# Optimization experiments

Measured on AMD Instinct MI355X. Metric: run time of the kernel, lower is better.

The kernel has to match this reference:

```python
import jax, jax.numpy as jnp
import numpy as np

B, Himg, Wimg, DIM = 8, 128, 128, 256
HEADS = 16            # d_head = DIM // HEADS = 16 == HEADS (required by temperature broadcast)
HW = Himg * Wimg


def setup_inputs() -> dict:
    key = jax.random.key(0)
    ks = jax.random.split(key, 9)
    s = 0.02
    return {
        "x": jax.random.normal(ks[0], (B, Himg, Wimg, DIM), jnp.float32),
        "w_qkv": jax.random.normal(ks[1], (DIM, 3 * DIM), jnp.float32) * s,
        "w_dw": jax.random.normal(ks[2], (3, 3, 1, 3 * DIM), jnp.float32) * s,  # HWIO, depthwise
        "w_out": jax.random.normal(ks[3], (DIM, DIM), jnp.float32) * s,
        "temperature": jnp.ones((1, 1, HEADS), jnp.float32),
        "mean_q": jax.random.normal(ks[4], (1, 1, HW, 1), jnp.float32) * 0.05,
        "var_q": 0.5 + jax.random.uniform(ks[5], (1, 1, HW, 1), jnp.float32),
        "mean_k": jax.random.normal(ks[6], (1, 1, HW, 1), jnp.float32) * 0.05,
        "var_k": 0.5 + jax.random.uniform(ks[7], (1, 1, HW, 1), jnp.float32),
    }


def _to_heads(t, b, hw, heads):
    # (b,h,w,heads*dh) -> (b, heads, h*w, dh)
    return t.reshape(b, hw, heads, -1).transpose(0, 2, 1, 3)


def reference(x, w_qkv, w_dw, w_out, temperature, mean_q, var_q, mean_k, var_k):
    b, h, w, c = x.shape
    heads = temperature.shape[-1]
    # pointwise QKV projection (1x1 conv, no bias)
    qkv = jnp.einsum('bhwc,cd->bhwd', x, w_qkv)
    # depthwise 3x3 conv, groups = 3*dim, 'same' padding
    qkv = jax.lax.conv_general_dilated(
        qkv, w_dw, window_strides=(1, 1), padding='SAME',
        dimension_numbers=('NHWC', 'HWIO', 'NHWC'),
        feature_group_count=3 * c)
    q, k, v = jnp.split(qkv, 3, axis=-1)
    q = _to_heads(q, b, h * w, heads)  # (b, heads, hw, dh)
    k = _to_heads(k, b, h * w, heads)
    v = _to_heads(v, b, h * w, heads)
    # keras Normalization(axis=-2): per-spatial-position mean/variance
    q = (q - mean_q) * jax.lax.rsqrt(var_q)
    k = (k - mean_k) * jax.lax.rsqrt(var_k)
    # channel attention: k^T @ q over spatial axis -> (b, heads, dh, dh)
    attn = jnp.einsum('bnsi,bnsj->bnij', k, q)
    attn = attn * temperature  # broadcasts over last axis (dh == heads)
    attn = jax.nn.softmax(attn, axis=-2)
    out = jnp.einsum('bnsd,bndj->bnsj', v, attn)  # v @ attn
    # (b, heads, hw, dh) -> (b, h, w, heads*dh)
    out = out.transpose(0, 2, 1, 3).reshape(b, h, w, c)
    out = jnp.einsum('bhwc,cd->bhwd', out, w_out)
    return out
```

## Files before the change

kernel.cpp:

```cpp
#include <hip/hip_runtime.h>
#include <cstdint>
#include <cstddef>

#define NB    8
#define HWSZ  16384
#define DIM   256
#define NCH   128
#define CHSZ  (HWSZ / NCH)

typedef short bf16x8 __attribute__((ext_vector_type(8)));
typedef float f32x4 __attribute__((ext_vector_type(4)));
typedef unsigned short u16;
typedef u16 u16x8 __attribute__((ext_vector_type(8)));

__device__ __forceinline__ float bf2f(u16 u) {
    union { uint32_t i; float f; } w; w.i = ((uint32_t)u) << 16; return w.f;
}
__device__ __forceinline__ u16 f2bf(float f) {
    union { float f; uint32_t i; } w; w.f = f;
    uint32_t x = w.i;
    return (u16)((x + 0x7fffu + ((x >> 16) & 1u)) >> 16);
}

__device__ __forceinline__ void gload_lds16(const u16* g, u16* l) {
    __builtin_amdgcn_global_load_lds(
        (const __attribute__((address_space(1))) uint32_t*)g,
        (__attribute__((address_space(3))) uint32_t*)l, 16, 0, 0);
}

__global__ void transpose_w32(const float* __restrict__ in, u16* __restrict__ out,
                              int K, int N) {
    int t = blockIdx.x * 256 + threadIdx.x;
    if (t < K * N) {
        int kk = t / N;
        int n  = t % N;
        out[(size_t)n * K + kk] = f2bf(in[t]);
    }
}

__global__ void conv_bf16(const float* __restrict__ in, u16* __restrict__ out,
                          int n8) {
    int t = blockIdx.x * 256 + threadIdx.x;
    if (t < n8) {
        const float4* p = (const float4*)(in + (size_t)t * 8);
        float4 a = p[0], b = p[1];
        u16x8 o;
        o[0] = f2bf(a.x); o[1] = f2bf(a.y); o[2] = f2bf(a.z); o[3] = f2bf(a.w);
        o[4] = f2bf(b.x); o[5] = f2bf(b.y); o[6] = f2bf(b.z); o[7] = f2bf(b.w);
        *(u16x8*)(out + (size_t)t * 8) = o;
    }
}

#define GEMM_BODY(STORE_STMT)                                                   \
    __shared__ u16 At[128 * 32];                                                \
    __shared__ u16 Bl[128 * 32];                                                \
    const int t    = threadIdx.x;                                               \
    const int lane = t & 63;                                                    \
    const int wave = t >> 6;                                                    \
    const int r16  = lane & 15;                                                 \
    const int quad = lane >> 4;                                                 \
    const int m0   = blockIdx.y * 128;                                          \
    const int n0   = blockIdx.x * 128;                                          \
    const int K    = 256;                                                       \
    const int wm   = (wave >> 1) * 64;                                          \
    const int wn   = (wave & 1) * 64;                                           \
    f32x4 acc[4][4];                                                            \
    _Pragma("unroll")                                                           \
    for (int mi = 0; mi < 4; ++mi)                                              \
        _Pragma("unroll")                                                       \
        for (int ni = 0; ni < 4; ++ni)                                          \
            acc[mi][ni] = (f32x4){0.f, 0.f, 0.f, 0.f};                          \
    const int srow = t >> 2;                \
    const int skc  = (t & 3) * 8;                         \
    for (int kk = 0; kk < K; kk += 32) {                                        \
        if (kk) __syncthreads();                                                \
        _Pragma("unroll")                                                       \
        for (int it = 0; it < 2; ++it) {                                        \
            int c   = t + it * 256;                                             \
            int row = srow + it * 64;                                           \
            gload_lds16(A  + (size_t)(m0 + row) * K + kk + skc, At + c * 8);    \
            gload_lds16(Bt + (size_t)(n0 + row) * K + kk + skc, Bl + c * 8);    \
        }                                                                       \
        __syncthreads();                                                        \
        bf16x8 af[4], bfr[4];                                                   \
        _Pragma("unroll")                                                       \
        for (int mi = 0; mi < 4; ++mi)                                          \
            af[mi] = *(const bf16x8*)(At + (wm + mi * 16 + r16) * 32 + quad * 8);\
        _Pragma("unroll")                                                       \
        for (int ni = 0; ni < 4; ++ni)                                          \
            bfr[ni] = *(const bf16x8*)(Bl + (wn + ni * 16 + r16) * 32 + quad * 8);\
        _Pragma("unroll")                                                       \
        for (int mi = 0; mi < 4; ++mi)                                          \
            _Pragma("unroll")                                                   \
            for (int ni = 0; ni < 4; ++ni)                                      \
                acc[mi][ni] = __builtin_amdgcn_mfma_f32_16x16x32_bf16(          \
                    af[mi], bfr[ni], acc[mi][ni], 0, 0, 0);                     \
    }                                                                           \
    _Pragma("unroll")                                                           \
    for (int mi = 0; mi < 4; ++mi)                                              \
        _Pragma("unroll")                                                       \
        for (int ni = 0; ni < 4; ++ni)                                          \
            _Pragma("unroll")                                                   \
            for (int r = 0; r < 4; ++r) {                                       \
                int m = m0 + wm + mi * 16 + quad * 4 + r;                       \
                int n = n0 + wn + ni * 16 + r16;                                \
                STORE_STMT;                                                     \
            }

__global__ __launch_bounds__(256) void gemm_lds_cbf(const u16* __restrict__ A,
                                                    const u16* __restrict__ Bt,
                                                    u16* __restrict__ C, int N) {
    GEMM_BODY(C[(size_t)m * N + n] = f2bf(acc[mi][ni][r]))
}

__global__ __launch_bounds__(256) void gemm_lds_cf32(const u16* __restrict__ A,
                                                     const u16* __restrict__ Bt,
                                                     float* __restrict__ C, int N) {
    GEMM_BODY(C[(size_t)m * N + n] = acc[mi][ni][r])
}

__global__ __launch_bounds__(192) void dwconv_norm(
        const u16* __restrict__ qkv, const float* __restrict__ wdw,
        const float* __restrict__ mq, const float* __restrict__ vq,
        const float* __restrict__ mk, const float* __restrict__ vk,
        u16* __restrict__ qo, u16* __restrict__ ko, u16* __restrict__ vo) {
    int t  = blockIdx.x * 192 + threadIdx.x;
    int g  = t % 96;
    int p  = t / 96;
    int c0 = g * 8;
    int b  = p >> 14;
    int s  = p & 16383;
    int y  = s >> 7;
    int x  = s & 127;

    float acc[8];
#pragma unroll
    for (int i = 0; i < 8; ++i) acc[i] = 0.f;

    for (int dy = -1; dy <= 1; ++dy) {
        int yy = y + dy;
        if (yy < 0 || yy > 127) continue;
        for (int dx = -1; dx <= 1; ++dx) {
            int xx = x + dx;
            if (xx < 0 || xx > 127) continue;
            const u16x8 in = *(const u16x8*)(qkv +
                ((size_t)b * HWSZ + yy * 128 + xx) * 768 + c0);
            const float* wp = wdw + (size_t)((dy + 1) * 3 + (dx + 1)) * 768 + c0;
            float4 w0 = *(const float4*)wp;
            float4 w1 = *(const float4*)(wp + 4);
            acc[0] += bf2f(in[0]) * w0.x; acc[1] += bf2f(in[1]) * w0.y;
            acc[2] += bf2f(in[2]) * w0.z; acc[3] += bf2f(in[3]) * w0.w;
            acc[4] += bf2f(in[4]) * w1.x; acc[5] += bf2f(in[5]) * w1.y;
            acc[6] += bf2f(in[6]) * w1.z; acc[7] += bf2f(in[7]) * w1.w;
        }
    }

    int seg = c0 >> 8;
    int cc  = c0 & 255;
    size_t op = (size_t)p * 256 + cc;
    u16x8 o;
    if (seg == 0) {
        float m = mq[s];
        float r = rsqrtf(vq[s]);
#pragma unroll
        for (int i = 0; i < 8; ++i) o[i] = f2bf((acc[i] - m) * r);
        *(u16x8*)(qo + op) = o;
    } else if (seg == 1) {
        float m = mk[s];
        float r = rsqrtf(vk[s]);
#pragma unroll
        for (int i = 0; i < 8; ++i) o[i] = f2bf((acc[i] - m) * r);
        *(u16x8*)(ko + op) = o;
    } else {
#pragma unroll
        for (int i = 0; i < 8; ++i) o[i] = f2bf(acc[i]);
        *(u16x8*)(vo + op) = o;
    }
}

__global__ __launch_bounds__(256) void attn_mfma(
        const u16* __restrict__ q, const u16* __restrict__ k,
        float* __restrict__ attn_ps, int nbn) {
    __shared__ u16 qt[32 * 256];
    __shared__ u16 kt[32 * 256];
    const int b    = blockIdx.x;
    const int ch   = blockIdx.y;
    const int t    = threadIdx.x;
    const int wave = t >> 6;
    const int lane = t & 63;
    const int r16  = lane & 15;
    const int quad = lane >> 4;
    const size_t base = (size_t)b * HWSZ * 256;
    const int sBeg = ch * CHSZ;

    f32x4 acc[4];
#pragma unroll
    for (int i = 0; i < 4; ++i) acc[i] = (f32x4){0.f, 0.f, 0.f, 0.f};

    for (int s0 = sBeg; s0 < sBeg + CHSZ; s0 += 32) {
        __syncthreads();
#pragma unroll
        for (int r = 0; r < 4; ++r) {
            int c   = t + r * 256;
            int row = c >> 5;
            int c32 = c & 31;
            int pcol = (c32 * 8) ^ ((row >> 3) << 4);
            *(u16x8*)(&qt[row * 256 + pcol]) =
                *(const u16x8*)(q + base + (size_t)(s0 + row) * 256 + c32 * 8);
            *(u16x8*)(&kt[row * 256 + pcol]) =
                *(const u16x8*)(k + base + (size_t)(s0 + row) * 256 + c32 * 8);
        }
        __syncthreads();
#pragma unroll
        for (int h4 = 0; h4 < 4; ++h4) {
            int h   = wave * 4 + h4;
            int pc  = (h * 16 + r16) ^ (quad << 4);
            u16x8 ak, aq;
#pragma unroll
            for (int e = 0; e < 8; ++e) {
                int addr = (quad * 8 + e) * 256 + pc;
                ak[e] = kt[addr];
                aq[e] = qt[addr];
            }
            acc[h4] = __builtin_amdgcn_mfma_f32_16x16x32_bf16(
                (bf16x8)ak, (bf16x8)aq, acc[h4], 0, 0, 0);
        }
    }

#pragma unroll
    for (int h4 = 0; h4 < 4; ++h4) {
        int h  = wave * 4 + h4;
        int bn = b * 16 + h;
#pragma unroll
        for (int r = 0; r < 4; ++r) {
            attn_ps[((size_t)ch * nbn + bn) * 256 + (quad * 4 + r) * 16 + r16] =
                acc[h4][r];
        }
    }
}

__global__ void reduce_attn(const float* __restrict__ ps,
                            float* __restrict__ out, int n) {
    int t = blockIdx.x * 256 + threadIdx.x;
    if (t < n) {
        float s = 0.f;
        for (int c = 0; c < NCH; ++c) s += ps[(size_t)c * n + t];
        out[t] = s;
    }
}

__global__ __launch_bounds__(64) void softmax_attn(
        const float* __restrict__ attn, const float* __restrict__ temp,
        float* __restrict__ attn_sm) {
    int bn = blockIdx.x;
    int j  = threadIdx.x;
    if (j >= 16) return;
    float tj = temp[j];
    float vals[16];
    float mx = -3.4e38f;
#pragma unroll
    for (int i = 0; i < 16; ++i) {
        vals[i] = attn[bn * 256 + i * 16 + j] * tj;
        mx = fmaxf(mx, vals[i]);
    }
    float sum = 0.f;
#pragma unroll
    for (int i = 0; i < 16; ++i) {
        vals[i] = expf(vals[i] - mx);
        sum += vals[i];
    }
    float inv = 1.f / sum;
#pragma unroll
    for (int i = 0; i < 16; ++i)
        attn_sm[bn * 256 + i * 16 + j] = vals[i] * inv;
}

__global__ __launch_bounds__(256) void apply_attn(
        const u16* __restrict__ v, const float* __restrict__ attn_sm,
        u16* __restrict__ out_mid) {
    __shared__ float alds[16 * 257];
    const int tid = threadIdx.x;
    const int t   = blockIdx.x * 256 + tid;
    const int n   = t & 15;
    const int p   = t >> 4;
    const int b   = p >> 14;

#pragma unroll
    for (int r = 0; r < 16; ++r) {
        int idx = r * 256 + tid;
        alds[(idx >> 8) * 257 + (idx & 255)] = attn_sm[(size_t)b * 4096 + idx];
    }
    __syncthreads();

    const u16* vp = v + (size_t)p * 256 + n * 16;
    u16x8 v0 = *(const u16x8*)vp;
    u16x8 v1 = *(const u16x8*)(vp + 8);
    float vv[16];
#pragma unroll
    for (int i = 0; i < 8; ++i) { vv[i] = bf2f(v0[i]); vv[8 + i] = bf2f(v1[i]); }

    const float* am = &alds[n * 257];
    float o[16];
#pragma unroll
    for (int j = 0; j < 16; ++j) o[j] = 0.f;
#pragma unroll
    for (int d = 0; d < 16; ++d) {
        float vd = vv[d];
#pragma unroll
        for (int j = 0; j < 16; ++j) o[j] += vd * am[d * 16 + j];
    }

    u16x8 o0, o1;
#pragma unroll
    for (int i = 0; i < 8; ++i) { o0[i] = f2bf(o[i]); o1[i] = f2bf(o[8 + i]); }
    u16* outp = out_mid + (size_t)p * 256 + n * 16;
    *(u16x8*)outp       = o0;
    *(u16x8*)(outp + 8) = o1;
}

extern "C" void kernel_launch(void* const* d_in, const int* in_sizes, int n_in,
                              void* d_out, int out_size, void* d_ws, size_t ws_size,
                              hipStream_t stream) {
    const float* x     = (const float*)d_in[0];
    const float* wqkv  = (const float*)d_in[1];
    const float* wdw   = (const float*)d_in[2];
    const float* wout  = (const float*)d_in[3];
    const float* temp  = (const float*)d_in[4];
    const float* mq    = (const float*)d_in[5];
    const float* vq    = (const float*)d_in[6];
    const float* mk    = (const float*)d_in[7];
    const float* vk    = (const float*)d_in[8];
    float* out_f = (float*)d_out;

    char* ws = (char*)d_ws;
    u16*   btq      = (u16*)ws;
    u16*   bto      = (u16*)(ws + 768 * 256 * 2);
    char*  dynb     = ws + 768 * 256 * 2 + 256 * 256 * 2;
    const size_t FIXED = (size_t)(768 * 256 * 2 + 256 * 256 * 2);

    const size_t PER_IMG = (size_t)HWSZ * 768 * 2 + 3 * (size_t)HWSZ * 256 * 2
                         + 2 * 4096 * 4;
    int CB = 8;
    while (CB > 1 && FIXED + (size_t)CB * PER_IMG > ws_size) CB >>= 1;

    transpose_w32<<<(256 * 768 + 255) / 256, 256, 0, stream>>>(wqkv, btq, 256, 768);
    transpose_w32<<<(256 * 256 + 255) / 256, 256, 0, stream>>>(wout, bto, 256, 256);

    const size_t QKVB = (size_t)CB * HWSZ * 768 * 2;
    const size_t SEGB = (size_t)CB * HWSZ * 256 * 2;
    u16*   qkv_c    = (u16*)dynb;
    u16*   qb       = (u16*)(dynb + QKVB);
    u16*   kb       = (u16*)(dynb + QKVB + SEGB);
    u16*   vb       = (u16*)(dynb + QKVB + 2 * SEGB);
    float* attn_raw = (float*)(dynb + QKVB + 3 * SEGB);
    float* attn_sm  = attn_raw + (size_t)CB * 4096;
    u16*   om_c     = qkv_c;
    u16*   xb       = qb;
    float* attn_ps  = (float*)qkv_c;

    const int rowsC = CB * HWSZ;
    const int nbn   = CB * 16;
    for (int b0 = 0; b0 < NB; b0 += CB) {
        const float* xc   = x + (size_t)b0 * HWSZ * 256;
        float*       outc = out_f + (size_t)b0 * HWSZ * 256;

        conv_bf16<<<(rowsC * 32 + 255) / 256, 256, 0, stream>>>(xc, xb, rowsC * 32);

        gemm_lds_cbf<<<dim3(768 / 128, rowsC / 128), 256, 0, stream>>>(xb, btq,
                                                                       qkv_c, 768);
        dwconv_norm<<<(rowsC * 96) / 192, 192, 0, stream>>>(qkv_c, wdw,
                                                            mq, vq, mk, vk,
                                                            qb, kb, vb);
        attn_mfma<<<dim3(CB, NCH), 256, 0, stream>>>(qb, kb, attn_ps, nbn);
        reduce_attn<<<(CB * 4096 + 255) / 256, 256, 0, stream>>>(attn_ps, attn_raw,
                                                                 CB * 4096);
        softmax_attn<<<CB * 16, 64, 0, stream>>>(attn_raw, temp, attn_sm);

        apply_attn<<<(rowsC * 16) / 256, 256, 0, stream>>>(vb, attn_sm, om_c);

        gemm_lds_cf32<<<dim3(256 / 128, rowsC / 128), 256, 0, stream>>>(om_c, bto,
                                                                        outc, 256);
    }
}
```

Before: 713.2 us.

## Tile depthwise conv over 4 output rows with register-cached weights

The depthwise 3x3 conv kernel now has each thread compute 4 vertically adjacent output pixels for 8 channels. It loads 6 input rows of 3 columns each, instead of 9 loads per output, and keeps all 9 weight taps in registers. This cuts redundant global and L2 reads of the bf16 qkv tensor and of the weights. The cost is more registers per thread, which a launch bound of 2 blocks per CU is meant to contain, and fewer blocks in the 3D grid. The edge loads clamp the row but not x-1 or x+1, so at x=0 or x=127 they may read neighbouring pixels or one element before the buffer before the values are masked to zero.

```diff
diff --git a/kernel.cpp b/kernel.cpp
--- a/kernel.cpp
+++ b/kernel.cpp
@@ -119,62 +119,91 @@
     GEMM_BODY(C[(size_t)m * N + n] = acc[mi][ni][r])
 }
 
-__global__ __launch_bounds__(192) void dwconv_norm(
+__global__ __launch_bounds__(192, 2) void dwconv_norm(
         const u16* __restrict__ qkv, const float* __restrict__ wdw,
         const float* __restrict__ mq, const float* __restrict__ vq,
         const float* __restrict__ mk, const float* __restrict__ vk,
         u16* __restrict__ qo, u16* __restrict__ ko, u16* __restrict__ vo) {
-    int t  = blockIdx.x * 192 + threadIdx.x;
-    int g  = t % 96;
-    int p  = t / 96;
-    int c0 = g * 8;
-    int b  = p >> 14;
-    int s  = p & 16383;
-    int y  = s >> 7;
-    int x  = s & 127;
-
-    float acc[8];
-#pragma unroll
-    for (int i = 0; i < 8; ++i) acc[i] = 0.f;
-
-    for (int dy = -1; dy <= 1; ++dy) {
-        int yy = y + dy;
-        if (yy < 0 || yy > 127) continue;
-        for (int dx = -1; dx <= 1; ++dx) {
-            int xx = x + dx;
-            if (xx < 0 || xx > 127) continue;
-            const u16x8 in = *(const u16x8*)(qkv +
-                ((size_t)b * HWSZ + yy * 128 + xx) * 768 + c0);
-            const float* wp = wdw + (size_t)((dy + 1) * 3 + (dx + 1)) * 768 + c0;
-            float4 w0 = *(const float4*)wp;
-            float4 w1 = *(const float4*)(wp + 4);
-            acc[0] += bf2f(in[0]) * w0.x; acc[1] += bf2f(in[1]) * w0.y;
-            acc[2] += bf2f(in[2]) * w0.z; acc[3] += bf2f(in[3]) * w0.w;
-            acc[4] += bf2f(in[4]) * w1.x; acc[5] += bf2f(in[5]) * w1.y;
-            acc[6] += bf2f(in[6]) * w1.z; acc[7] += bf2f(in[7]) * w1.w;
-        }
-    }
-
-    int seg = c0 >> 8;
-    int cc  = c0 & 255;
-    size_t op = (size_t)p * 256 + cc;
-    u16x8 o;
-    if (seg == 0) {
-        float m = mq[s];
-        float r = rsqrtf(vq[s]);
-#pragma unroll
-        for (int i = 0; i < 8; ++i) o[i] = f2bf((acc[i] - m) * r);
-        *(u16x8*)(qo + op) = o;
-    } else if (seg == 1) {
-        float m = mk[s];
-        float r = rsqrtf(vk[s]);
-#pragma unroll
-        for (int i = 0; i < 8; ++i) o[i] = f2bf((acc[i] - m) * r);
-        *(u16x8*)(ko + op) = o;
-    } else {
-#pragma unroll
-        for (int i = 0; i < 8; ++i) o[i] = f2bf(acc[i]);
-        *(u16x8*)(vo + op) = o;
+    const int t    = threadIdx.x;
+    const int g    = t % 96;
+    const int c0   = g * 8;
+    const int xcol = t / 96;
+    const int x    = blockIdx.x * 2 + xcol;
+    const int y0   = blockIdx.y * 4;
+    const int b    = blockIdx.z;
+
+    float w[9][8];
+#pragma unroll
+    for (int kt = 0; kt < 9; ++kt) {
+        float4 w0 = *(const float4*)(wdw + (size_t)kt * 768 + c0);
+        float4 w1 = *(const float4*)(wdw + (size_t)kt * 768 + c0 + 4);
+        w[kt][0] = w0.x; w[kt][1] = w0.y; w[kt][2] = w0.z; w[kt][3] = w0.w;
+        w[kt][4] = w1.x; w[kt][5] = w1.y; w[kt][6] = w1.z; w[kt][7] = w1.w;
+    }
+
+    float acc[4][8];
+#pragma unroll
+    for (int r = 0; r < 4; ++r)
+#pragma unroll
+        for (int c = 0; c < 8; ++c) acc[r][c] = 0.f;
+
+    const bool xlok = (x > 0);
+    const bool xrok = (x < 127);
+    const u16x8 vz = {0, 0, 0, 0, 0, 0, 0, 0};
+
+#pragma unroll
+    for (int i = 0; i < 6; ++i) {
+        const int  rowy = y0 - 1 + i;
+        const bool rok  = (unsigned)rowy < 128u;
+        const int  rowc = rowy < 0 ? 0 : (rowy > 127 ? 127 : rowy);
+        const u16* rp = qkv + ((size_t)b * HWSZ + rowc * 128 + x) * 768 + c0;
+        u16x8 a0 = *(const u16x8*)(rp - 768);
+        u16x8 a1 = *(const u16x8*)(rp);
+        u16x8 a2 = *(const u16x8*)(rp + 768);
+        if (!(rok && xlok)) a0 = vz;
+        if (!rok)           a1 = vz;
+        if (!(rok && xrok)) a2 = vz;
+        float f0[8], f1[8], f2[8];
+#pragma unroll
+        for (int c = 0; c < 8; ++c) {
+            f0[c] = bf2f(a0[c]); f1[c] = bf2f(a1[c]); f2[c] = bf2f(a2[c]);
+        }
+#pragma unroll
+        for (int r = 0; r < 4; ++r) {
+            if (r < i - 2 || r > i) continue;
+            const int tr = (i - r) * 3;
+#pragma unroll
+            for (int c = 0; c < 8; ++c) {
+                acc[r][c] += f0[c] * w[tr + 0][c];
+                acc[r][c] += f1[c] * w[tr + 1][c];
+                acc[r][c] += f2[c] * w[tr + 2][c];
+            }
+        }
+    }
+
+    const int seg = c0 >> 8;
+    const int cc  = c0 & 255;
+#pragma unroll
+    for (int r = 0; r < 4; ++r) {
+        const int    s  = (y0 + r) * 128 + x;
+        const size_t p  = (size_t)b * HWSZ + s;
+        const size_t op = p * 256 + cc;
+        u16x8 o;
+        if (seg == 0) {
+            float m = mq[s], rs = rsqrtf(vq[s]);
+#pragma unroll
+            for (int c = 0; c < 8; ++c) o[c] = f2bf((acc[r][c] - m) * rs);
+            *(u16x8*)(qo + op) = o;
+        } else if (seg == 1) {
+            float m = mk[s], rs = rsqrtf(vk[s]);
+#pragma unroll
+            for (int c = 0; c < 8; ++c) o[c] = f2bf((acc[r][c] - m) * rs);
+            *(u16x8*)(ko + op) = o;
+        } else {
+#pragma unroll
+            for (int c = 0; c < 8; ++c) o[c] = f2bf(acc[r][c]);
+            *(u16x8*)(vo + op) = o;
+        }
     }
 }
 
@@ -368,9 +397,9 @@
 
         gemm_lds_cbf<<<dim3(768 / 128, rowsC / 128), 256, 0, stream>>>(xb, btq,
                                                                        qkv_c, 768);
-        dwconv_norm<<<(rowsC * 96) / 192, 192, 0, stream>>>(qkv_c, wdw,
-                                                            mq, vq, mk, vk,
-                                                            qb, kb, vb);
+        dwconv_norm<<<dim3(64, 32, CB), 192, 0, stream>>>(qkv_c, wdw,
+                                                          mq, vq, mk, vk,
+                                                          qb, kb, vb);
         attn_mfma<<<dim3(CB, NCH), 256, 0, stream>>>(qb, kb, attn_ps, nbn);
         reduce_attn<<<(CB * 4096 + 255) / 256, 256, 0, stream>>>(attn_ps, attn_raw,
                                                                  CB * 4096);
```

Result: faster. 631.7 us (-11.4%).
